# Kernel tuning notes

Measured on AMD Instinct MI355X. Metric: run time of the kernel, lower is better.

The kernel has to match this reference:

```python
import jax, jax.numpy as jnp
import numpy as np

N, IN_DIM, OUT_DIM, HEADS = 8192, 256, 128, 2


def setup_inputs() -> dict:
    key = jax.random.key(0)
    k1, k2, k3, k4, k5 = jax.random.split(key, 5)
    features = jax.random.normal(k1, (N, IN_DIM), dtype=jnp.float32)
    adjacency = jax.random.randint(k2, (N, N), 0, 2, dtype=jnp.int32)
    # nn.Linear(input_dim, output_dim*heads, bias=False): weight [out, in]
    W = jax.random.normal(k3, (OUT_DIM * HEADS, IN_DIM), dtype=jnp.float32) * 0.05
    attn_src = jax.random.normal(k4, (HEADS, OUT_DIM), dtype=jnp.float32) * 0.05
    attn_dst = jax.random.normal(k5, (HEADS, OUT_DIM), dtype=jnp.float32) * 0.05
    return {"features": features, "adjacency": adjacency, "W": W,
            "attn_src": attn_src, "attn_dst": attn_dst}


def reference(features, adjacency, W, attn_src, attn_dst):
    n = features.shape[0]
    # transformed: [N, H, F]
    transformed = (features @ W.T).reshape(n, HEADS, OUT_DIM)
    src_scores = jnp.einsum('nhf,hf->nh', transformed, attn_src)  # [N, H]
    dst_scores = jnp.einsum('nhf,hf->nh', transformed, attn_dst)  # [N, H]
    # logits: [N_src, N_dst, H]
    logits = jax.nn.leaky_relu(src_scores[:, None, :] + dst_scores[None, :, :],
                               negative_slope=0.2)
    mask = adjacency > 0  # [N, N]
    logits = jnp.where(mask[:, :, None], logits, -jnp.inf)
    attention = jax.nn.softmax(logits, axis=1)  # softmax over dst dim (dim=1)
    attention = jnp.nan_to_num(attention, nan=0.0, posinf=0.0, neginf=0.0)
    aggregated = jnp.einsum('ijh,jhf->ihf', attention, transformed)  # [N, H, F]
    return aggregated.mean(axis=1)  # [N, F]
```

## Files before the change

### kernel.cpp

```cpp
#include <hip/hip_runtime.h>
#include <stdint.h>
#include <stddef.h>

#define NN 8192
#define KD 256
#define CD 256
#define FD 128
#define BI 32
#define BJ 32

typedef __attribute__((ext_vector_type(4))) float f32x4;
typedef __attribute__((ext_vector_type(8))) short b16x8;

__device__ __forceinline__ unsigned short f2bf(float x) {
    unsigned int u = __float_as_uint(x);
    u += 0x7fffu + ((u >> 16) & 1u);
    return (unsigned short)(u >> 16);
}

__device__ __forceinline__ void async16(const void* g, void* l) {
    __builtin_amdgcn_global_load_lds(
        (const __attribute__((address_space(1))) unsigned int*)g,
        (__attribute__((address_space(3))) unsigned int*)l, 16, 0, 0);
}

__device__ __forceinline__ float exp_pack_store(
    const int4 a0, const int4 a1, const float4 d0, const float4 d1,
    float sv, unsigned short* wdst)
{
    const int am[8] = {a0.x, a0.y, a0.z, a0.w, a1.x, a1.y, a1.z, a1.w};
    const float dd[8] = {d0.x, d0.y, d0.z, d0.w, d1.x, d1.y, d1.z, d1.w};
    const float ninf = __int_as_float(0xff800000);
    float e[8]; float dp = 0.f;
#pragma unroll
    for (int k = 0; k < 8; ++k) {
        float x = sv + dd[k];
        x = fmaxf(x, 0.f) + 0.2f * fminf(x, 0.f);
        x = am[k] != 0 ? x : ninf;
        const float ev = __expf(x);
        dp += ev; e[k] = ev;
    }
    union { unsigned short us[8]; b16x8 v; } pk;
#if __has_builtin(__builtin_amdgcn_cvt_pk_bf16_f32)
#pragma unroll
    for (int k = 0; k < 4; ++k) {
        auto p = __builtin_amdgcn_cvt_pk_bf16_f32(e[2 * k], e[2 * k + 1]);
        __builtin_memcpy(&pk.us[2 * k], &p, 4);
    }
#else
#pragma unroll
    for (int k = 0; k < 8; ++k) pk.us[k] = f2bf(e[k]);
#endif
    *(b16x8*)wdst = pk.v;
    return dp;
}

__global__ __launch_bounds__(256) void k_transform(
    const float* __restrict__ feat, const float* __restrict__ W,
    const float* __restrict__ asrc, const float* __restrict__ adst,
    unsigned short* __restrict__ Tt, float* __restrict__ s_t, float* __restrict__ d_t)
{
    __shared__ unsigned short a_lds[64 * 32];
    __shared__ unsigned short b_lds[256 * 32];
    __shared__ unsigned short tr_lds[256 * 72];
    __shared__ float sc_lds[4][64];
    __shared__ float dc_lds[4][64];

    const int t = threadIdx.x;
    const int wave = t >> 6, lane = t & 63;
    const int l15 = lane & 15, quad = lane >> 4;
    const int n0 = blockIdx.x * 64;
    const int ai = t >> 2, ag = t & 3;

    f32x4 acc[4][4] = {};
    for (int kc = 0; kc < 8; ++kc) {
        const int k0 = kc * 32;
        __syncthreads();
        {
            const float* src = feat + (size_t)(n0 + ai) * KD + k0 + ag * 8;
            const float4 v0 = *(const float4*)src;
            const float4 v1 = *(const float4*)(src + 4);
            union { unsigned short us[8]; b16x8 v; } pk;
            pk.us[0] = f2bf(v0.x); pk.us[1] = f2bf(v0.y);
            pk.us[2] = f2bf(v0.z); pk.us[3] = f2bf(v0.w);
            pk.us[4] = f2bf(v1.x); pk.us[5] = f2bf(v1.y);
            pk.us[6] = f2bf(v1.z); pk.us[7] = f2bf(v1.w);
            const int slot = ag ^ ((ai >> 1) & 3);
            *(b16x8*)&a_lds[ai * 32 + slot * 8] = pk.v;
        }
        for (int p = 0; p < 4; ++p) {
            const int G = p * 256 + t;
            const int c = G >> 2, g = G & 3;
            const float* src = W + (size_t)c * KD + k0 + g * 8;
            const float4 v0 = *(const float4*)src;
            const float4 v1 = *(const float4*)(src + 4);
            union { unsigned short us[8]; b16x8 v; } pk;
            pk.us[0] = f2bf(v0.x); pk.us[1] = f2bf(v0.y);
            pk.us[2] = f2bf(v0.z); pk.us[3] = f2bf(v0.w);
            pk.us[4] = f2bf(v1.x); pk.us[5] = f2bf(v1.y);
            pk.us[6] = f2bf(v1.z); pk.us[7] = f2bf(v1.w);
            const int slot = g ^ ((c >> 1) & 3);
            *(b16x8*)&b_lds[c * 32 + slot * 8] = pk.v;
        }
        __syncthreads();
        b16x8 af[4], bfr[4];
        for (int mt = 0; mt < 4; ++mt) {
            const int m = mt * 16 + l15;
            af[mt] = *(const b16x8*)&a_lds[m * 32 + (quad ^ ((m >> 1) & 3)) * 8];
        }
        for (int nt = 0; nt < 4; ++nt) {
            const int c = wave * 64 + nt * 16 + l15;
            bfr[nt] = *(const b16x8*)&b_lds[c * 32 + (quad ^ ((c >> 1) & 3)) * 8];
        }
        for (int mt = 0; mt < 4; ++mt)
            for (int nt = 0; nt < 4; ++nt)
                acc[mt][nt] = __builtin_amdgcn_mfma_f32_16x16x32_bf16(
                    af[mt], bfr[nt], acc[mt][nt], 0, 0, 0);
    }

    float aS[4], aD[4];
    for (int nt = 0; nt < 4; ++nt) {
        const int c = wave * 64 + nt * 16 + l15;
        aS[nt] = asrc[c]; aD[nt] = adst[c];
    }
    for (int mt = 0; mt < 4; ++mt)
        for (int r = 0; r < 4; ++r) {
            float vs = 0.f, vd = 0.f;
            for (int nt = 0; nt < 4; ++nt) {
                const float x = acc[mt][nt][r];
                vs += x * aS[nt]; vd += x * aD[nt];
            }
            vs += __shfl_xor(vs, 1); vd += __shfl_xor(vd, 1);
            vs += __shfl_xor(vs, 2); vd += __shfl_xor(vd, 2);
            vs += __shfl_xor(vs, 4); vd += __shfl_xor(vd, 4);
            vs += __shfl_xor(vs, 8); vd += __shfl_xor(vd, 8);
            if (l15 == 0) {
                const int nl = mt * 16 + quad * 4 + r;
                sc_lds[wave][nl] = vs; dc_lds[wave][nl] = vd;
            }
        }
    for (int mt = 0; mt < 4; ++mt)
        for (int nt = 0; nt < 4; ++nt)
            for (int r = 0; r < 4; ++r) {
                const int c = wave * 64 + nt * 16 + l15;
                const int n = mt * 16 + quad * 4 + r;
                tr_lds[c * 72 + n] = f2bf(acc[mt][nt][r]);
            }
    __syncthreads();
    if (t < 128) {
        const int n = t >> 1, h = t & 1;
        s_t[(size_t)h * NN + n0 + n] = sc_lds[h * 2][n] + sc_lds[h * 2 + 1][n];
        d_t[(size_t)h * NN + n0 + n] = dc_lds[h * 2][n] + dc_lds[h * 2 + 1][n];
    }
    for (int p = 0; p < 8; ++p) {
        const int idx = p * 256 + t;
        const int c = idx >> 3, g = idx & 7;
        *(b16x8*)(Tt + (size_t)c * NN + n0 + g * 8) = *(const b16x8*)&tr_lds[c * 72 + g * 8];
    }
}

__global__ __launch_bounds__(256, 4) void k_gat(
    const int* __restrict__ adj, const unsigned short* __restrict__ Tt,
    const float* __restrict__ s_t, const float* __restrict__ d_t,
    float* __restrict__ num_part,
    float* __restrict__ den_part,
    int njt)
{
    __shared__ unsigned short tt_lds[2][256 * 32];
    __shared__ unsigned short w_lds[2][2][32][32];

    const int t = threadIdx.x;
    const int wave = t >> 6, lane = t & 63;
    const int l15 = lane & 15, quad = lane >> 4;
    const int i0 = blockIdx.x * BI;
    const int chunk = blockIdx.y;
    const size_t jbase = (size_t)chunk * njt * BJ;

    const int eh = t >> 7;
    const int wi = (t & 127) >> 2;
    const int g4 = t & 3;
    const int gi = i0 + wi;
    const float sv = s_t[(size_t)eh * NN + gi];
    const int wslot = (g4 ^ ((wi >> 1) & 3)) * 8;

    const int mh = wave >> 1, fh = wave & 1;
    const int cbase = mh * 128 + fh * 64;

    f32x4 acc[2][4] = {};
    float den = 0.f;

    const int* ap = adj + (size_t)gi * NN + jbase + g4 * 8;
    const float* dp_ = d_t + (size_t)eh * NN + jbase + g4 * 8;

    for (int p = 0; p < 4; ++p) {
        const int G = (p * 4 + wave) * 64 + lane;
        const int c = G >> 2;
        const int g = (G & 3) ^ ((c >> 1) & 3);
        async16(Tt + (size_t)c * NN + jbase + g * 8,
                (char*)&tt_lds[0][0] + (size_t)(p * 4 + wave) * 1024);
    }
    __builtin_amdgcn_sched_barrier(0);
    int4 cA0 = ((const int4*)ap)[0], cA1 = ((const int4*)ap)[1];
    float4 cD0 = ((const float4*)dp_)[0], cD1 = ((const float4*)dp_)[1];
    {
        const int j1 = (njt > 1) ? BJ : 0;
        int4 nA0 = *(const int4*)(ap + j1);
        int4 nA1 = *(const int4*)(ap + j1 + 4);
        float4 nD0 = *(const float4*)(dp_ + j1);
        float4 nD1 = *(const float4*)(dp_ + j1 + 4);
        den += exp_pack_store(cA0, cA1, cD0, cD1, sv, &w_lds[0][eh][wi][wslot]);
        cA0 = nA0; cA1 = nA1; cD0 = nD0; cD1 = nD1;
    }
    asm volatile("s_waitcnt vmcnt(4) lgkmcnt(0)\n\ts_barrier" ::: "memory");

    for (int jt = 0; jt < njt; ++jt) {
        const int cur = jt & 1, nxt = cur ^ 1;
        b16x8 af[2], bfr[4];
        for (int mt = 0; mt < 2; ++mt) {
            const int m = mt * 16 + l15;
            af[mt] = *(const b16x8*)&w_lds[cur][mh][m][(quad ^ ((m >> 1) & 3)) * 8];
        }
        for (int nt = 0; nt < 4; ++nt) {
            const int c = cbase + nt * 16 + l15;
            bfr[nt] = *(const b16x8*)&tt_lds[cur][c * 32 + (quad ^ ((c >> 1) & 3)) * 8];
        }
        const size_t jnext = jbase + (size_t)((jt + 1 < njt) ? jt + 1 : jt) * BJ;
        for (int p = 0; p < 4; ++p) {
            const int G = (p * 4 + wave) * 64 + lane;
            const int c = G >> 2;
            const int g = (G & 3) ^ ((c >> 1) & 3);
            async16(Tt + (size_t)c * NN + jnext + g * 8,
                    (char*)&tt_lds[nxt][0] + (size_t)(p * 4 + wave) * 1024);
        }
        __builtin_amdgcn_sched_barrier(0);
        const int j2 = (((jt + 2 < njt) ? jt + 2 : njt - 1)) * BJ;
        int4 nA0 = *(const int4*)(ap + j2);
        int4 nA1 = *(const int4*)(ap + j2 + 4);
        float4 nD0 = *(const float4*)(dp_ + j2);
        float4 nD1 = *(const float4*)(dp_ + j2 + 4);
        const float dpv = exp_pack_store(cA0, cA1, cD0, cD1, sv,
                                         &w_lds[nxt][eh][wi][wslot]);
        if (jt + 1 < njt) den += dpv;
        for (int mt = 0; mt < 2; ++mt)
            for (int nt = 0; nt < 4; ++nt)
                acc[mt][nt] = __builtin_amdgcn_mfma_f32_16x16x32_bf16(
                    af[mt], bfr[nt], acc[mt][nt], 0, 0, 0);
        cA0 = nA0; cA1 = nA1; cD0 = nD0; cD1 = nD1;
        asm volatile("s_waitcnt vmcnt(4) lgkmcnt(0)\n\ts_barrier" ::: "memory");
    }

    float dv = den;
    dv += __shfl_xor(dv, 1); dv += __shfl_xor(dv, 2);
    if (g4 == 0)
        den_part[((size_t)chunk * 2 + eh) * NN + gi] = dv;

    float* np_ = num_part + (size_t)chunk * NN * CD;
    for (int mt = 0; mt < 2; ++mt)
        for (int nt = 0; nt < 4; ++nt)
            for (int r = 0; r < 4; ++r) {
                const int n = i0 + mt * 16 + quad * 4 + r;
                const int c = cbase + nt * 16 + l15;
                np_[(size_t)n * CD + c] = acc[mt][nt][r];
            }
}

__global__ __launch_bounds__(256) void k_combine(
    const float* __restrict__ num_part, const float* __restrict__ den_part,
    float* __restrict__ out, int jsplit)
{
    const int idx = blockIdx.x * 256 + threadIdx.x;
    const int n = idx >> 7, f = idx & 127;
    const size_t row = (size_t)n * CD;
    float n0 = 0.f, n1 = 0.f, d0 = 0.f, d1 = 0.f;
    for (int c = 0; c < jsplit; ++c) {
        const size_t base = (size_t)c * NN * CD;
        n0 += num_part[base + row + f];
        n1 += num_part[base + row + 128 + f];
        d0 += den_part[((size_t)c * 2 + 0) * NN + n];
        d1 += den_part[((size_t)c * 2 + 1) * NN + n];
    }
    const float r0 = d0 != 0.f ? n0 / d0 : 0.f;
    const float r1 = d1 != 0.f ? n1 / d1 : 0.f;
    out[idx] = 0.5f * (r0 + r1);
}

extern "C" void kernel_launch(void* const* d_in, const int* in_sizes, int n_in,
                              void* d_out, int out_size, void* d_ws, size_t ws_size,
                              hipStream_t stream) {
    const float* feat = (const float*)d_in[0];
    const int*   adj  = (const int*)d_in[1];
    const float* W    = (const float*)d_in[2];
    const float* asrc = (const float*)d_in[3];
    const float* adst = (const float*)d_in[4];
    float* out = (float*)d_out;

    const int jsplit = (ws_size >= ((size_t)40 << 20)) ? 4 : 2;
    const int njt = (NN / jsplit) / BJ;

    char* ws = (char*)d_ws;
    unsigned short* Tt = (unsigned short*)ws;
    float* s_t  = (float*)(ws + ((size_t)4 << 20));
    float* d_t  = (float*)(ws + ((size_t)4 << 20) + (64 << 10));
    float* den  = (float*)(ws + ((size_t)4 << 20) + (128 << 10));
    float* nump = (float*)(ws + ((size_t)8 << 20));

    k_transform<<<128, 256, 0, stream>>>(feat, W, asrc, adst, Tt, s_t, d_t);
    k_gat<<<dim3(NN / BI, jsplit), 256, 0, stream>>>(adj, Tt, s_t, d_t, nump, den, njt);
    k_combine<<<NN * FD / 256, 256, 0, stream>>>(nump, den, out, jsplit);
}
```

Before: 479.9 us.

## Pre-pack adjacency into a bitmask in the front kernel and consume bits in the GAT kernel

Result: slower. 506.2 us (+5.5%).

```diff
diff --git a/kernel.cpp b/kernel.cpp
--- a/kernel.cpp
+++ b/kernel.cpp
@@ -8,6 +8,7 @@
 #define FD 128
 #define BI 32
 #define BJ 32
+#define PACK_BLOCKS 1024
 
 typedef __attribute__((ext_vector_type(4))) float f32x4;
 typedef __attribute__((ext_vector_type(8))) short b16x8;
@@ -25,10 +26,8 @@
 }
 
 __device__ __forceinline__ float exp_pack_store(
-    const int4 a0, const int4 a1, const float4 d0, const float4 d1,
-    float sv, unsigned short* wdst)
+    int m8, const float4 d0, const float4 d1, float sv, unsigned short* wdst)
 {
-    const int am[8] = {a0.x, a0.y, a0.z, a0.w, a1.x, a1.y, a1.z, a1.w};
     const float dd[8] = {d0.x, d0.y, d0.z, d0.w, d1.x, d1.y, d1.z, d1.w};
     const float ninf = __int_as_float(0xff800000);
     float e[8]; float dp = 0.f;
@@ -36,7 +35,7 @@
     for (int k = 0; k < 8; ++k) {
         float x = sv + dd[k];
         x = fmaxf(x, 0.f) + 0.2f * fminf(x, 0.f);
-        x = am[k] != 0 ? x : ninf;
+        x = (m8 & (1 << k)) ? x : ninf;
         const float ev = __expf(x);
         dp += ev; e[k] = ev;
     }
@@ -55,9 +54,10 @@
     return dp;
 }
 
-__global__ __launch_bounds__(256) void k_transform(
+__global__ __launch_bounds__(256) void k_front(
     const float* __restrict__ feat, const float* __restrict__ W,
     const float* __restrict__ asrc, const float* __restrict__ adst,
+    const int* __restrict__ adj, unsigned int* __restrict__ mask,
     unsigned short* __restrict__ Tt, float* __restrict__ s_t, float* __restrict__ d_t)
 {
     __shared__ unsigned short a_lds[64 * 32];
@@ -67,6 +67,26 @@
     __shared__ float dc_lds[4][64];
 
     const int t = threadIdx.x;
+
+    if (blockIdx.x >= 128) {
+        const int pb = blockIdx.x - 128;
+        const size_t base = (size_t)pb * 16384;
+        const int4* a4 = (const int4*)adj;
+#pragma unroll 4
+        for (int st = 0; st < 64; ++st) {
+            const size_t i4 = base + (size_t)st * 256 + t;
+            const int4 v = a4[i4];
+            unsigned int nib = (v.x != 0 ? 1u : 0u) | (v.y != 0 ? 2u : 0u) |
+                               (v.z != 0 ? 4u : 0u) | (v.w != 0 ? 8u : 0u);
+            unsigned int wd = nib << (4 * (t & 7));
+            wd |= __shfl_xor(wd, 1);
+            wd |= __shfl_xor(wd, 2);
+            wd |= __shfl_xor(wd, 4);
+            if ((t & 7) == 0) mask[i4 >> 3] = wd;
+        }
+        return;
+    }
+
     const int wave = t >> 6, lane = t & 63;
     const int l15 = lane & 15, quad = lane >> 4;
     const int n0 = blockIdx.x * 64;
@@ -160,7 +180,7 @@
 }
 
 __global__ __launch_bounds__(256, 4) void k_gat(
-    const int* __restrict__ adj, const unsigned short* __restrict__ Tt,
+    const unsigned char* __restrict__ maskb, const unsigned short* __restrict__ Tt,
     const float* __restrict__ s_t, const float* __restrict__ d_t,
     float* __restrict__ num_part,
     float* __restrict__ den_part,
@@ -189,7 +209,7 @@
     f32x4 acc[2][4] = {};
     float den = 0.f;
 
-    const int* ap = adj + (size_t)gi * NN + jbase + g4 * 8;
+    const unsigned char* mrow = maskb + (size_t)gi * (NN / 8) + (jbase >> 3) + g4;
     const float* dp_ = d_t + (size_t)eh * NN + jbase + g4 * 8;
 
     for (int p = 0; p < 4; ++p) {
@@ -200,18 +220,17 @@
                 (char*)&tt_lds[0][0] + (size_t)(p * 4 + wave) * 1024);
     }
     __builtin_amdgcn_sched_barrier(0);
-    int4 cA0 = ((const int4*)ap)[0], cA1 = ((const int4*)ap)[1];
+    int cM = mrow[0];
     float4 cD0 = ((const float4*)dp_)[0], cD1 = ((const float4*)dp_)[1];
     {
-        const int j1 = (njt > 1) ? BJ : 0;
-        int4 nA0 = *(const int4*)(ap + j1);
-        int4 nA1 = *(const int4*)(ap + j1 + 4);
-        float4 nD0 = *(const float4*)(dp_ + j1);
-        float4 nD1 = *(const float4*)(dp_ + j1 + 4);
-        den += exp_pack_store(cA0, cA1, cD0, cD1, sv, &w_lds[0][eh][wi][wslot]);
-        cA0 = nA0; cA1 = nA1; cD0 = nD0; cD1 = nD1;
-    }
-    asm volatile("s_waitcnt vmcnt(4) lgkmcnt(0)\n\ts_barrier" ::: "memory");
+        const int j1 = (njt > 1) ? 1 : 0;
+        int nM = mrow[j1 * 4];
+        float4 nD0 = *(const float4*)(dp_ + j1 * BJ);
+        float4 nD1 = *(const float4*)(dp_ + j1 * BJ + 4);
+        den += exp_pack_store(cM, cD0, cD1, sv, &w_lds[0][eh][wi][wslot]);
+        cM = nM; cD0 = nD0; cD1 = nD1;
+    }
+    asm volatile("s_waitcnt vmcnt(3) lgkmcnt(0)\n\ts_barrier" ::: "memory");
 
     for (int jt = 0; jt < njt; ++jt) {
         const int cur = jt & 1, nxt = cur ^ 1;
@@ -233,20 +252,19 @@
                     (char*)&tt_lds[nxt][0] + (size_t)(p * 4 + wave) * 1024);
         }
         __builtin_amdgcn_sched_barrier(0);
-        const int j2 = (((jt + 2 < njt) ? jt + 2 : njt - 1)) * BJ;
-        int4 nA0 = *(const int4*)(ap + j2);
-        int4 nA1 = *(const int4*)(ap + j2 + 4);
-        float4 nD0 = *(const float4*)(dp_ + j2);
-        float4 nD1 = *(const float4*)(dp_ + j2 + 4);
-        const float dpv = exp_pack_store(cA0, cA1, cD0, cD1, sv,
+        const int j2 = ((jt + 2 < njt) ? jt + 2 : njt - 1);
+        int nM = mrow[j2 * 4];
+        float4 nD0 = *(const float4*)(dp_ + j2 * BJ);
+        float4 nD1 = *(const float4*)(dp_ + j2 * BJ + 4);
+        const float dpv = exp_pack_store(cM, cD0, cD1, sv,
                                          &w_lds[nxt][eh][wi][wslot]);
         if (jt + 1 < njt) den += dpv;
         for (int mt = 0; mt < 2; ++mt)
             for (int nt = 0; nt < 4; ++nt)
                 acc[mt][nt] = __builtin_amdgcn_mfma_f32_16x16x32_bf16(
                     af[mt], bfr[nt], acc[mt][nt], 0, 0, 0);
-        cA0 = nA0; cA1 = nA1; cD0 = nD0; cD1 = nD1;
-        asm volatile("s_waitcnt vmcnt(4) lgkmcnt(0)\n\ts_barrier" ::: "memory");
+        cM = nM; cD0 = nD0; cD1 = nD1;
+        asm volatile("s_waitcnt vmcnt(3) lgkmcnt(0)\n\ts_barrier" ::: "memory");
     }
 
     float dv = den;
@@ -294,7 +312,7 @@
     const float* adst = (const float*)d_in[4];
     float* out = (float*)d_out;
 
-    const int jsplit = (ws_size >= ((size_t)40 << 20)) ? 4 : 2;
+    const int jsplit = (ws_size >= ((size_t)45 << 20)) ? 4 : 2;
     const int njt = (NN / jsplit) / BJ;
 
     char* ws = (char*)d_ws;
@@ -302,9 +320,12 @@
     float* s_t  = (float*)(ws + ((size_t)4 << 20));
     float* d_t  = (float*)(ws + ((size_t)4 << 20) + (64 << 10));
     float* den  = (float*)(ws + ((size_t)4 << 20) + (128 << 10));
-    float* nump = (float*)(ws + ((size_t)8 << 20));
-
-    k_transform<<<128, 256, 0, stream>>>(feat, W, asrc, adst, Tt, s_t, d_t);
-    k_gat<<<dim3(NN / BI, jsplit), 256, 0, stream>>>(adj, Tt, s_t, d_t, nump, den, njt);
+    unsigned int* mask = (unsigned int*)(ws + ((size_t)5 << 20));
+    float* nump = (float*)(ws + ((size_t)13 << 20));
+
+    k_front<<<128 + PACK_BLOCKS, 256, 0, stream>>>(feat, W, asrc, adst, adj,
+                                                   mask, Tt, s_t, d_t);
+    k_gat<<<dim3(NN / BI, jsplit), 256, 0, stream>>>((const unsigned char*)mask,
+                                                     Tt, s_t, d_t, nump, den, njt);
     k_combine<<<NN * FD / 256, 256, 0, stream>>>(nump, den, out, jsplit);
 }
```
